# Performance work log

Hardware: AMD Instinct MI355X
Metric: run time of the kernel (lower is better)

Reference implementation:

```python
import jax, jax.numpy as jnp
import numpy as np

C = 1024
H = 16
HS = C // H
HID = 4096
A_MIX = 0.7
B_MIX = 0.3
EPS = 1e-5


def layernorm(x, w, b):
    mu = jnp.mean(x, axis=-1, keepdims=True)
    var = jnp.mean(jnp.square(x - mu), axis=-1, keepdims=True)
    return (x - mu) * jax.lax.rsqrt(var + EPS) * w + b


def setup_inputs() -> dict:
    key = jax.random.key(0)
    ks = jax.random.split(key, 12)
    B, N = 4, 1024
    s = 1.0 / np.sqrt(C)
    sh = 1.0 / np.sqrt(HID)
    return {
        "x": jax.random.normal(ks[0], (B, N, C), jnp.float32),
        "Query": jax.random.normal(ks[1], (B, H, N, HS), jnp.float32),
        "Key": jax.random.normal(ks[2], (B, H, N, HS), jnp.float32),
        "Value": jax.random.normal(ks[3], (B, H, N, HS), jnp.float32),
        "ln_w": jnp.ones((C,), jnp.float32),
        "ln_b": jnp.zeros((C,), jnp.float32),
        "qk_w": jax.random.normal(ks[4], (2 * C, C), jnp.float32) * s,
        "qk_b": jnp.zeros((2 * C,), jnp.float32),
        "v_w": jax.random.normal(ks[5], (C, C), jnp.float32) * s,
        "v_b": jnp.zeros((C,), jnp.float32),
        "out_w": jax.random.normal(ks[6], (C, C), jnp.float32) * s,
        "out_b": jnp.zeros((C,), jnp.float32),
        "mlp_w1": jax.random.normal(ks[7], (HID, C), jnp.float32) * s,
        "mlp_b1": jnp.zeros((HID,), jnp.float32),
        "mlp_w2": jax.random.normal(ks[8], (C, HID), jnp.float32) * sh,
        "mlp_b2": jnp.zeros((C,), jnp.float32),
    }


def reference(x, Query, Key, Value, ln_w, ln_b, qk_w, qk_b, v_w, v_b,
              out_w, out_b, mlp_w1, mlp_b1, mlp_w2, mlp_b2):
    B, N, _ = x.shape
    x1 = x
    xn = layernorm(x, ln_w, ln_b)
    # qk projection -> view (B,N,H,HS,2), permute -> (2,B,H,N,HS)
    qk = (xn @ qk_w.T + qk_b).reshape(B, N, H, HS, 2)
    Q = jnp.transpose(qk[..., 0], (0, 2, 1, 3))  # (B,H,N,HS)
    K = jnp.transpose(qk[..., 1], (0, 2, 1, 3))
    V = jnp.transpose((xn @ v_w.T + v_b).reshape(B, N, H, HS), (0, 2, 1, 3))
    Query = A_MIX * Q + B_MIX * Query
    Key = A_MIX * K + B_MIX * Key
    Value = B_MIX * Value + A_MIX * V
    attn = jnp.einsum('bhqd,bhkd->bhqk', Query, Key) / np.sqrt(HS)
    attn = jax.nn.softmax(attn, axis=-1)  # dropout = identity in eval
    o = jnp.einsum('bhqk,bhkd->bhqd', attn, Value)
    o = jnp.transpose(o, (0, 2, 1, 3)).reshape(B, N, C)
    o = o @ out_w.T + out_b
    x = x1 + o
    x2 = x
    xn2 = layernorm(x, ln_w, ln_b)  # same layernorm params reused
    h = jax.nn.gelu(xn2 @ mlp_w1.T + mlp_b1, approximate=False)
    m = h @ mlp_w2.T + mlp_b2
    return (m + x2, Query, Key, Value)
```

## Files before the change

### kernel.cpp

```cpp
#include <hip/hip_runtime.h>

using bf16x8 = __attribute__((ext_vector_type(8))) __bf16;
using f32x4  = __attribute__((ext_vector_type(4))) float;

#define AS1(p) (const __attribute__((address_space(1))) void*)(p)
#define AS3(p) (__attribute__((address_space(3))) void*)(p)

__device__ __forceinline__ unsigned short f2bf(float f) {
    unsigned int u = __float_as_uint(f);
    unsigned int r = (u + 0x7FFFu + ((u >> 16) & 1u)) >> 16;
    return (unsigned short)r;
}
__device__ __forceinline__ float bf2f(unsigned short u) {
    return __uint_as_float((unsigned int)u << 16);
}

__global__ __launch_bounds__(256) void cvt_kernel(const float* __restrict__ in,
                                                  unsigned short* __restrict__ out,
                                                  int n) {
    int i = (blockIdx.x * 256 + threadIdx.x) * 4;
    if (i < n) {
        float4 v = *(const float4*)(in + i);
        ushort4 o = make_ushort4(f2bf(v.x), f2bf(v.y), f2bf(v.z), f2bf(v.w));
        *(ushort4*)(out + i) = o;
    }
}

__global__ __launch_bounds__(256) void ln_kernel(const float* __restrict__ in,
                                                 const float* __restrict__ w,
                                                 const float* __restrict__ b,
                                                 unsigned short* __restrict__ out) {
    const int row = blockIdx.x;
    const int tid = threadIdx.x;
    const float4 v = *(const float4*)(in + (size_t)row * 1024 + tid * 4);
    float s  = v.x + v.y + v.z + v.w;
    float ss = v.x * v.x + v.y * v.y + v.z * v.z + v.w * v.w;
    #pragma unroll
    for (int m = 1; m < 64; m <<= 1) {
        s  += __shfl_xor(s, m, 64);
        ss += __shfl_xor(ss, m, 64);
    }
    __shared__ float red[8];
    if ((tid & 63) == 0) { red[(tid >> 6) * 2] = s; red[(tid >> 6) * 2 + 1] = ss; }
    __syncthreads();
    s  = red[0] + red[2] + red[4] + red[6];
    ss = red[1] + red[3] + red[5] + red[7];
    const float mu  = s * (1.0f / 1024.0f);
    const float var = ss * (1.0f / 1024.0f) - mu * mu;
    const float rstd = rsqrtf(var + 1e-5f);
    const float4 wv = *(const float4*)(w + tid * 4);
    const float4 bv = *(const float4*)(b + tid * 4);
    ushort4 o;
    o.x = f2bf((v.x - mu) * rstd * wv.x + bv.x);
    o.y = f2bf((v.y - mu) * rstd * wv.y + bv.y);
    o.z = f2bf((v.z - mu) * rstd * wv.z + bv.z);
    o.w = f2bf((v.w - mu) * rstd * wv.w + bv.w);
    *(ushort4*)(out + (size_t)row * 1024 + tid * 4) = o;
}

template <int EPI>
__global__ __launch_bounds__(256, 2)
void gemm_bt(const unsigned short* __restrict__ A,
             const unsigned short* __restrict__ W,
             const float* __restrict__ bias,
             int M, int N, int K,
             const float* __restrict__ e0, const float* __restrict__ e1,
             float* __restrict__ o0, float* __restrict__ o1,
             unsigned short* __restrict__ u0, unsigned short* __restrict__ u1) {
    __shared__ unsigned short As[128 * 128];
    __shared__ unsigned short Bs[128 * 128];
    const int tid  = threadIdx.x;
    const int wave = tid >> 6, lane = tid & 63;
    const int wr = wave >> 1, wc = wave & 1;
    const int q15 = lane & 15, g = lane >> 4;

    const int gx = gridDim.x;
    const int nwg = gx * gridDim.y;
    int flat = blockIdx.y * gx + blockIdx.x;
    flat = (flat & 7) * (nwg >> 3) + (flat >> 3);
    const int gm0 = (flat / gx) * 128, gn0 = (flat % gx) * 128;

    f32x4 acc[4][4] = {};

    const int lrow4 = lane >> 4;
    const int lslot = lane & 15;
    const int rswz  = q15 << 4;

    for (int k0 = 0; k0 < K; k0 += 128) {
        #pragma unroll
        for (int i = 0; i < 8; ++i) {
            const int row  = wave * 32 + i * 4 + lrow4;
            const int selm = (lslot ^ (row & 15)) << 3;
            __builtin_amdgcn_global_load_lds(AS1(A + (size_t)(gm0 + row) * K + k0 + selm),
                                             AS3((char*)As + wave * 8192 + i * 1024), 16, 0, 0);
            __builtin_amdgcn_global_load_lds(AS1(W + (size_t)(gn0 + row) * K + k0 + selm),
                                             AS3((char*)Bs + wave * 8192 + i * 1024), 16, 0, 0);
        }
        __syncthreads();
        #pragma unroll
        for (int kk = 0; kk < 4; ++kk) {
            bf16x8 af[4], bfr[4];
            #pragma unroll
            for (int m = 0; m < 4; ++m)
                af[m] = *(const bf16x8*)((char*)As + (wr * 64 + m * 16 + q15) * 256 +
                                         ((kk * 64 + g * 16) ^ rswz));
            #pragma unroll
            for (int n = 0; n < 4; ++n)
                bfr[n] = *(const bf16x8*)((char*)Bs + (wc * 64 + n * 16 + q15) * 256 +
                                          ((kk * 64 + g * 16) ^ rswz));
            #pragma unroll
            for (int m = 0; m < 4; ++m)
                #pragma unroll
                for (int n = 0; n < 4; ++n)
                    acc[m][n] = __builtin_amdgcn_mfma_f32_16x16x32_bf16(af[m], bfr[n], acc[m][n], 0, 0, 0);
        }
        __syncthreads();
    }

    #pragma unroll
    for (int m = 0; m < 4; ++m)
    #pragma unroll
    for (int n = 0; n < 4; ++n)
    #pragma unroll
    for (int j = 0; j < 4; ++j) {
        const int r = gm0 + wr * 64 + m * 16 + g * 4 + j;
        const int c = gn0 + wc * 64 + n * 16 + q15;
        const float val = acc[m][n][j] + bias[c];
        if constexpr (EPI == 0) {
            const int bb = r >> 10, nn = r & 1023;
            const int h = c >> 7, hs = (c >> 1) & 63, isk = c & 1;
            const size_t idx = (((size_t)(bb * 16 + h)) * 1024 + nn) * 64 + hs;
            if (!isk) { const float mx = 0.7f * val + 0.3f * e0[idx]; o0[idx] = mx; u0[idx] = f2bf(mx); }
            else      { const float mx = 0.7f * val + 0.3f * e1[idx]; o1[idx] = mx; u1[idx] = f2bf(mx); }
        } else if constexpr (EPI == 1) {
            const int bb = r >> 10, nn = r & 1023;
            const int h = c >> 6, hs = c & 63;
            const size_t idx = (((size_t)(bb * 16 + h)) * 1024 + nn) * 64 + hs;
            const float mx = 0.7f * val + 0.3f * e0[idx];
            o0[idx] = mx;
            u0[(((size_t)(bb * 16 + h)) * 64 + hs) * 1024 + nn] = f2bf(mx);
        } else if constexpr (EPI == 2) {
            const size_t idx = (size_t)r * N + c;
            o0[idx] = val + e0[idx];
        } else if constexpr (EPI == 3) {
            const float gg = 0.5f * val * (1.0f + erff(val * 0.70710678118f));
            u0[(size_t)r * N + c] = f2bf(gg);
        } else {
            const size_t idx = (size_t)r * N + c;
            o0[idx] = val + e0[idx];
        }
    }
}

__global__ __launch_bounds__(256, 6)
void attn_kernel(const unsigned short* __restrict__ Qb,
                 const unsigned short* __restrict__ Kb,
                 const unsigned short* __restrict__ Vt,
                 unsigned short* __restrict__ Op,
                 float* __restrict__ Mws,
                 float* __restrict__ Lws) {
    const int bh = blockIdx.y;
    const int z  = blockIdx.z;
    const int tid = threadIdx.x, wave = tid >> 6, lane = tid & 63;
    const int qbase = blockIdx.x * 64 + wave * 16;
    const int q15 = lane & 15, g = lane >> 4;

    const unsigned short* Qh = Qb + (size_t)bh * 1024 * 64;
    const unsigned short* Kh = Kb + (size_t)bh * 1024 * 64;
    const unsigned short* Vh = Vt + (size_t)bh * 64 * 1024;

    __shared__ alignas(128) unsigned short Ks[64 * 64];
    __shared__ alignas(128) unsigned short Vs[64 * 64];
    __shared__ alignas(128) unsigned short Ps[4][1024];
    char* const Pb = (char*)Ps[wave] + q15 * 128;
    const int swz = (q15 & 7) << 4;

    const int srow8 = lane >> 3;
    const int selm  = (((lane & 7) ^ srow8) << 3);

    bf16x8 aq[2];
    aq[0] = *(const bf16x8*)&Qh[(size_t)(qbase + q15) * 64 + 0  + g * 8];
    aq[1] = *(const bf16x8*)&Qh[(size_t)(qbase + q15) * 64 + 32 + g * 8];

    f32x4 o[4] = {};
    float mrow = -1e30f, lrow = 0.f;

    const int t0 = z * 8;
    for (int t = t0; t < t0 + 8; ++t) {
        const int kb = t * 64;
        #pragma unroll
        for (int i = 0; i < 2; ++i) {
            const int r = wave * 16 + i * 8 + srow8;
            __builtin_amdgcn_global_load_lds(AS1(Kh + (size_t)(kb + r) * 64 + selm),
                                             AS3((char*)Ks + wave * 2048 + i * 1024), 16, 0, 0);
            __builtin_amdgcn_global_load_lds(AS1(Vh + (size_t)r * 1024 + kb + selm),
                                             AS3((char*)Vs + wave * 2048 + i * 1024), 16, 0, 0);
        }
        __syncthreads();

        f32x4 s[4] = {};
        #pragma unroll
        for (int kt = 0; kt < 4; ++kt) {
            #pragma unroll
            for (int kk = 0; kk < 2; ++kk) {
                const bf16x8 bk = *(const bf16x8*)((char*)Ks + (kt * 16 + q15) * 128 +
                                                   ((kk * 64 + g * 16) ^ swz));
                s[kt] = __builtin_amdgcn_mfma_f32_16x16x32_bf16(bk, aq[kk], s[kt], 0, 0, 0);
            }
        }
        float pm = -1e30f;
        #pragma unroll
        for (int kt = 0; kt < 4; ++kt) {
            s[kt] *= 0.125f;
            pm = fmaxf(pm, fmaxf(fmaxf(s[kt][0], s[kt][1]), fmaxf(s[kt][2], s[kt][3])));
        }
        pm = fmaxf(pm, __shfl_xor(pm, 16, 64));
        pm = fmaxf(pm, __shfl_xor(pm, 32, 64));
        const float mnew = fmaxf(mrow, pm);
        const float alpha = __expf(mrow - mnew);
        mrow = mnew;

        float rs = 0.f;
        #pragma unroll
        for (int kt = 0; kt < 4; ++kt) {
            const float p0 = __expf(s[kt][0] - mnew);
            const float p1 = __expf(s[kt][1] - mnew);
            const float p2 = __expf(s[kt][2] - mnew);
            const float p3 = __expf(s[kt][3] - mnew);
            rs += (p0 + p1) + (p2 + p3);
            uint2 pk;
            pk.x = (unsigned int)f2bf(p0) | ((unsigned int)f2bf(p1) << 16);
            pk.y = (unsigned int)f2bf(p2) | ((unsigned int)f2bf(p3) << 16);
            *(uint2*)(Pb + (((kt * 32 + g * 8) ^ swz))) = pk;
        }
        rs += __shfl_xor(rs, 16, 64);
        rs += __shfl_xor(rs, 32, 64);
        lrow = lrow * alpha + rs;

        float af[4];
        #pragma unroll
        for (int j = 0; j < 4; ++j) af[j] = __shfl(alpha, g * 4 + j, 64);
        #pragma unroll
        for (int dt = 0; dt < 4; ++dt)
            #pragma unroll
            for (int j = 0; j < 4; ++j) o[dt][j] *= af[j];

        #pragma unroll
        for (int Bb = 0; Bb < 2; ++Bb) {
            const bf16x8 pa = *(const bf16x8*)(Pb + (((Bb * 64 + g * 16) ^ swz)));
            #pragma unroll
            for (int dt = 0; dt < 4; ++dt) {
                const bf16x8 vb = *(const bf16x8*)((char*)Vs + (dt * 16 + q15) * 128 +
                                                   ((Bb * 64 + g * 16) ^ swz));
                o[dt] = __builtin_amdgcn_mfma_f32_16x16x32_bf16(pa, vb, o[dt], 0, 0, 0);
            }
        }
        __syncthreads();
    }

    #pragma unroll
    for (int dt = 0; dt < 4; ++dt)
        #pragma unroll
        for (int j = 0; j < 4; ++j) {
            const int q = qbase + g * 4 + j;
            Op[(((size_t)z * 64 + bh) * 1024 + q) * 64 + dt * 16 + q15] = f2bf(o[dt][j]);
        }
    if (g == 0) {
        const size_t mi = ((size_t)z * 64 + bh) * 1024 + qbase + q15;
        Mws[mi] = mrow;
        Lws[mi] = lrow;
    }
}

__global__ __launch_bounds__(256)
void attn_combine(const unsigned short* __restrict__ Op,
                  const float* __restrict__ Mws,
                  const float* __restrict__ Lws,
                  unsigned short* __restrict__ Ob) {
    const int e4 = blockIdx.x * 256 + threadIdx.x;
    const int d0 = (e4 & 15) * 4;
    const int q  = (e4 >> 4) & 1023;
    const int bh = e4 >> 14;
    const size_t base0 = (((size_t)bh) * 1024 + q) * 64 + d0;
    const size_t base1 = (((size_t)(64 + bh)) * 1024 + q) * 64 + d0;
    const ushort4 a = *(const ushort4*)&Op[base0];
    const ushort4 c = *(const ushort4*)&Op[base1];
    const size_t mi0 = (size_t)bh * 1024 + q;
    const size_t mi1 = mi0 + 64 * 1024;
    const float m0 = Mws[mi0], m1 = Mws[mi1];
    const float l0 = Lws[mi0], l1 = Lws[mi1];
    const float m  = fmaxf(m0, m1);
    const float w0 = __expf(m0 - m), w1 = __expf(m1 - m);
    const float inv = 1.0f / (l0 * w0 + l1 * w1);
    ushort4 r;
    r.x = f2bf((bf2f(a.x) * w0 + bf2f(c.x) * w1) * inv);
    r.y = f2bf((bf2f(a.y) * w0 + bf2f(c.y) * w1) * inv);
    r.z = f2bf((bf2f(a.z) * w0 + bf2f(c.z) * w1) * inv);
    r.w = f2bf((bf2f(a.w) * w0 + bf2f(c.w) * w1) * inv);
    const int b = bh >> 4, h = bh & 15;
    *(ushort4*)&Ob[((size_t)(b * 1024 + q)) * 1024 + h * 64 + d0] = r;
}

extern "C" void kernel_launch(void* const* d_in, const int* in_sizes, int n_in,
                              void* d_out, int out_size, void* d_ws, size_t ws_size,
                              hipStream_t stream) {
    (void)in_sizes; (void)n_in; (void)out_size; (void)ws_size;
    const float* x     = (const float*)d_in[0];
    const float* Qin   = (const float*)d_in[1];
    const float* Kin   = (const float*)d_in[2];
    const float* Vin   = (const float*)d_in[3];
    const float* ln_w  = (const float*)d_in[4];
    const float* ln_b  = (const float*)d_in[5];
    const float* qk_w  = (const float*)d_in[6];
    const float* qk_b  = (const float*)d_in[7];
    const float* v_w   = (const float*)d_in[8];
    const float* v_b   = (const float*)d_in[9];
    const float* out_w = (const float*)d_in[10];
    const float* out_b = (const float*)d_in[11];
    const float* w1    = (const float*)d_in[12];
    const float* b1    = (const float*)d_in[13];
    const float* w2    = (const float*)d_in[14];
    const float* b2    = (const float*)d_in[15];

    const size_t FOUR_M = (size_t)4 * 1024 * 1024;
    float* out0 = (float*)d_out;
    float* Qout = out0 + FOUR_M;
    float* Kout = Qout + FOUR_M;
    float* Vout = Kout + FOUR_M;

    char* ws = (char*)d_ws;
    const size_t MB = 1024 * 1024;
    unsigned short* xn   = (unsigned short*)(ws + 0);
    unsigned short* qkwb = (unsigned short*)(ws + 8 * MB);
    unsigned short* vwb  = (unsigned short*)(ws + 12 * MB);
    unsigned short* owb  = (unsigned short*)(ws + 14 * MB);
    unsigned short* w1b  = (unsigned short*)(ws + 16 * MB);
    unsigned short* w2b  = (unsigned short*)(ws + 24 * MB);
    unsigned short* Qbuf = (unsigned short*)(ws + 32 * MB);
    unsigned short* Kbuf = (unsigned short*)(ws + 40 * MB);
    unsigned short* Vtb  = (unsigned short*)(ws + 48 * MB);
    unsigned short* atto = (unsigned short*)(ws + 56 * MB);
    unsigned short* hbuf = (unsigned short*)(ws + 32 * MB);
    float* y1 = (float*)(ws + 64 * MB);
    unsigned short* Oprt = (unsigned short*)(ws + 64 * MB);
    float* Mws = (float*)(ws + 8 * MB);
    float* Lws = (float*)(ws + 8 * MB + 512 * 1024);

    cvt_kernel<<<2048, 256, 0, stream>>>(qk_w, qkwb, 2048 * 1024);
    cvt_kernel<<<1024, 256, 0, stream>>>(v_w,  vwb,  1024 * 1024);
    cvt_kernel<<<1024, 256, 0, stream>>>(out_w, owb, 1024 * 1024);
    cvt_kernel<<<4096, 256, 0, stream>>>(w1, w1b, 4096 * 1024);
    cvt_kernel<<<4096, 256, 0, stream>>>(w2, w2b, 4096 * 1024);

    ln_kernel<<<4096, 256, 0, stream>>>(x, ln_w, ln_b, xn);

    {
        dim3 g(2048 / 128, 4096 / 128);
        gemm_bt<0><<<g, 256, 0, stream>>>(xn, qkwb, qk_b, 4096, 2048, 1024,
                                          Qin, Kin, Qout, Kout, Qbuf, Kbuf);
    }
    {
        dim3 g(1024 / 128, 4096 / 128);
        gemm_bt<1><<<g, 256, 0, stream>>>(xn, vwb, v_b, 4096, 1024, 1024,
                                          Vin, nullptr, Vout, nullptr, Vtb, nullptr);
    }
    {
        dim3 g(16, 64, 2);
        attn_kernel<<<g, 256, 0, stream>>>(Qbuf, Kbuf, Vtb, Oprt, Mws, Lws);
        attn_combine<<<4096, 256, 0, stream>>>(Oprt, Mws, Lws, atto);
    }
    {
        dim3 g(1024 / 128, 4096 / 128);
        gemm_bt<2><<<g, 256, 0, stream>>>(atto, owb, out_b, 4096, 1024, 1024,
                                          x, nullptr, y1, nullptr, nullptr, nullptr);
    }
    ln_kernel<<<4096, 256, 0, stream>>>(y1, ln_w, ln_b, xn);
    {
        dim3 g(4096 / 128, 4096 / 128);
        gemm_bt<3><<<g, 256, 0, stream>>>(xn, w1b, b1, 4096, 4096, 1024,
                                          nullptr, nullptr, nullptr, nullptr, hbuf, nullptr);
    }
    {
        dim3 g(1024 / 128, 4096 / 128);
        gemm_bt<4><<<g, 256, 0, stream>>>(hbuf, w2b, b2, 4096, 1024, 4096,
                                          y1, nullptr, out0, nullptr, nullptr, nullptr);
    }
}
```

Baseline: 278.7 us.

## Use 256x256-tile GEMM with fast tanh-GELU for MLP up-projection

```diff
diff --git a/kernel.cpp b/kernel.cpp
--- a/kernel.cpp
+++ b/kernel.cpp
@@ -13,6 +13,10 @@
 }
 __device__ __forceinline__ float bf2f(unsigned short u) {
     return __uint_as_float((unsigned int)u << 16);
+}
+__device__ __forceinline__ float gelu_fast(float x) {
+    const float a = 1.5957691f * (x + 0.044715f * x * x * x);
+    return x / (1.0f + __expf(-a));
 }
 
 __global__ __launch_bounds__(256) void cvt_kernel(const float* __restrict__ in,
@@ -142,13 +146,78 @@
         } else if constexpr (EPI == 2) {
             const size_t idx = (size_t)r * N + c;
             o0[idx] = val + e0[idx];
-        } else if constexpr (EPI == 3) {
-            const float gg = 0.5f * val * (1.0f + erff(val * 0.70710678118f));
-            u0[(size_t)r * N + c] = f2bf(gg);
         } else {
             const size_t idx = (size_t)r * N + c;
             o0[idx] = val + e0[idx];
         }
+    }
+}
+
+__global__ __launch_bounds__(512, 1)
+void gemm_big_gelu(const unsigned short* __restrict__ A,
+                   const unsigned short* __restrict__ W,
+                   const float* __restrict__ bias,
+                   int M, int N, int K,
+                   unsigned short* __restrict__ u0) {
+    __shared__ unsigned short As[256 * 64];
+    __shared__ unsigned short Bs[256 * 64];
+    const int tid  = threadIdx.x;
+    const int wave = tid >> 6, lane = tid & 63;
+    const int wr = wave >> 2, wc = wave & 3;
+    const int q15 = lane & 15, g = lane >> 4;
+
+    const int gx = gridDim.x;
+    const int nwg = gx * gridDim.y;
+    int flat = blockIdx.y * gx + blockIdx.x;
+    flat = (flat & 7) * (nwg >> 3) + (flat >> 3);
+    const int gm0 = (flat / gx) * 256, gn0 = (flat % gx) * 256;
+
+    f32x4 acc[8][4] = {};
+
+    const int srow8 = lane >> 3;
+    const int selm  = (((lane & 7) ^ srow8) << 3);
+    const int rswz  = (q15 & 7) << 4;
+
+    for (int k0 = 0; k0 < K; k0 += 64) {
+        #pragma unroll
+        for (int i = 0; i < 4; ++i) {
+            const int row = i * 64 + wave * 8 + srow8;
+            __builtin_amdgcn_global_load_lds(AS1(A + (size_t)(gm0 + row) * K + k0 + selm),
+                                             AS3((char*)As + (i * 64 + wave * 8) * 128), 16, 0, 0);
+            __builtin_amdgcn_global_load_lds(AS1(W + (size_t)(gn0 + row) * K + k0 + selm),
+                                             AS3((char*)Bs + (i * 64 + wave * 8) * 128), 16, 0, 0);
+        }
+        __syncthreads();
+        #pragma unroll
+        for (int kk = 0; kk < 2; ++kk) {
+            bf16x8 af[8], bfr[4];
+            #pragma unroll
+            for (int m = 0; m < 8; ++m)
+                af[m] = *(const bf16x8*)((char*)As + (wr * 128 + m * 16 + q15) * 128 +
+                                         ((kk * 64 + g * 16) ^ rswz));
+            #pragma unroll
+            for (int n = 0; n < 4; ++n)
+                bfr[n] = *(const bf16x8*)((char*)Bs + (wc * 64 + n * 16 + q15) * 128 +
+                                          ((kk * 64 + g * 16) ^ rswz));
+            #pragma unroll
+            for (int m = 0; m < 8; ++m)
+                #pragma unroll
+                for (int n = 0; n < 4; ++n)
+                    acc[m][n] = __builtin_amdgcn_mfma_f32_16x16x32_bf16(af[m], bfr[n], acc[m][n], 0, 0, 0);
+        }
+        __syncthreads();
+    }
+
+    #pragma unroll
+    for (int m = 0; m < 8; ++m)
+    #pragma unroll
+    for (int n = 0; n < 4; ++n)
+    #pragma unroll
+    for (int j = 0; j < 4; ++j) {
+        const int r = gm0 + wr * 128 + m * 16 + g * 4 + j;
+        const int c = gn0 + wc * 64 + n * 16 + q15;
+        const float val = acc[m][n][j] + bias[c];
+        u0[(size_t)r * N + c] = f2bf(gelu_fast(val));
     }
 }
 
@@ -376,9 +445,8 @@
     }
     ln_kernel<<<4096, 256, 0, stream>>>(y1, ln_w, ln_b, xn);
     {
-        dim3 g(4096 / 128, 4096 / 128);
-        gemm_bt<3><<<g, 256, 0, stream>>>(xn, w1b, b1, 4096, 4096, 1024,
-                                          nullptr, nullptr, nullptr, nullptr, hbuf, nullptr);
+        dim3 g(4096 / 256, 4096 / 256);
+        gemm_big_gelu<<<g, 512, 0, stream>>>(xn, w1b, b1, 4096, 4096, 1024, hbuf);
     }
     {
         dim3 g(1024 / 128, 4096 / 128);
```

New measurement: 266.9 us. 1.04x faster.
